# Kernel tuning notes

Hardware: AMD Instinct MI355X
Metric: run time of the kernel (lower is better)

The kernel has to match this reference:

```python
import jax, jax.numpy as jnp
import numpy as np

B, T, F = 256, 512, 256
H, C = 1024, 128


def setup_inputs() -> dict:
    key = jax.random.key(0)
    ks = jax.random.split(key, 12)
    s = 0.05
    return {
        "y": jax.random.normal(ks[0], (B, T, F), jnp.float32),
        "W_ih1": jax.random.normal(ks[1], (4 * H, F), jnp.float32) * s,
        "W_hh1": jax.random.normal(ks[2], (4 * H, H), jnp.float32) * s,
        "b_ih1": jax.random.normal(ks[3], (4 * H,), jnp.float32) * s,
        "b_hh1": jax.random.normal(ks[4], (4 * H,), jnp.float32) * s,
        "W_ih2": jax.random.normal(ks[5], (4 * H, H), jnp.float32) * s,
        "W_hh2": jax.random.normal(ks[6], (4 * H, H), jnp.float32) * s,
        "b_ih2": jax.random.normal(ks[7], (4 * H,), jnp.float32) * s,
        "b_hh2": jax.random.normal(ks[8], (4 * H,), jnp.float32) * s,
        "W_out": jax.random.normal(ks[9], (C, H), jnp.float32) * s,
        "b_out": jax.random.normal(ks[10], (C,), jnp.float32) * s,
    }


def _lstm_cell(x, h, c, W_ih, W_hh, b_ih, b_hh):
    # PyTorch LSTMCell: gates ordered i, f, g, o
    gates = x @ W_ih.T + b_ih + h @ W_hh.T + b_hh
    i, f, g, o = jnp.split(gates, 4, axis=-1)
    i, f, o = jax.nn.sigmoid(i), jax.nn.sigmoid(f), jax.nn.sigmoid(o)
    g = jnp.tanh(g)
    c_new = f * c + i * g
    h_new = o * jnp.tanh(c_new)
    return h_new, c_new


def reference(y, W_ih1, W_hh1, b_ih1, b_hh1, W_ih2, W_hh2, b_ih2, b_hh2, W_out, b_out):
    n = y.shape[0]
    z = jnp.zeros((n, H), jnp.float32)

    def step(carry, x_t):
        h1, c1, h2, c2 = carry
        h1, c1 = _lstm_cell(x_t, h1, c1, W_ih1, W_hh1, b_ih1, b_hh1)
        h2, c2 = _lstm_cell(h1, h2, c2, W_ih2, W_hh2, b_ih2, b_hh2)
        h2 = jnp.tanh(h2)  # note: tanh'd h2 is also the recurrent state, as in source
        out = jax.nn.relu(h2 @ W_out.T + b_out)
        return (h1, c1, h2, c2), out

    xs = jnp.transpose(y, (1, 0, 2))  # [T, B, F]
    _, outs = jax.lax.scan(step, (z, z, z, z), xs)
    # return_sequences=False -> last timestep output [B, C]
    return outs[-1]
```

## Files before the change

### kernel.cpp

```cpp
#include <hip/hip_runtime.h>
#include <hip/hip_bf16.h>

#define Bb 256
#define Tt 512
#define Ff 256
#define Hh 1024
#define Cc 128
#define NBLK 256
#define NTHR 512

typedef __bf16 bf16;
typedef bf16 bf16x8 __attribute__((ext_vector_type(8)));
typedef float f32x4 __attribute__((ext_vector_type(4)));

#define MFMA(a, b, c) __builtin_amdgcn_mfma_f32_16x16x32_bf16(a, b, c, 0, 0, 0)

struct SMem {
    bf16x8 w[2 * 64 * 64];
    bf16 hstage[256 * 8];
};

__device__ __forceinline__ float fsig(float x) {
    x = fminf(30.f, fmaxf(-30.f, x));
    return __builtin_amdgcn_rcpf(1.f + __expf(-x));
}
__device__ __forceinline__ float ftanh(float x) {
    x = fminf(15.f, fmaxf(-15.f, x));
    float e = __expf(2.f * x);
    return (e - 1.f) * __builtin_amdgcn_rcpf(e + 1.f);
}

#define STX4_SC1(p, v) \
    asm volatile("global_store_dwordx4 %0, %1, off sc1" :: "v"(p), "v"(v) : "memory")
#define LDX4_PLAIN(dst, base, OFF) \
    asm volatile("global_load_dwordx4 %0, %1, off offset:" #OFF : "=v"(dst) : "v"(base))

#define ISSUE_CHUNK(B0, B1, P0, P1) do { \
    LDX4_PLAIN(B0[0], (P0), 0);   LDX4_PLAIN(B0[1], (P0), 64);  LDX4_PLAIN(B0[2], (P0), 128); LDX4_PLAIN(B0[3], (P0), 192); \
    LDX4_PLAIN(B0[4], (P0), 256); LDX4_PLAIN(B0[5], (P0), 320); LDX4_PLAIN(B0[6], (P0), 384); LDX4_PLAIN(B0[7], (P0), 448); \
    LDX4_PLAIN(B1[0], (P1), 0);   LDX4_PLAIN(B1[1], (P1), 64);  LDX4_PLAIN(B1[2], (P1), 128); LDX4_PLAIN(B1[3], (P1), 192); \
    LDX4_PLAIN(B1[4], (P1), 256); LDX4_PLAIN(B1[5], (P1), 320); LDX4_PLAIN(B1[6], (P1), 384); LDX4_PLAIN(B1[7], (P1), 448); \
} while (0)

#define WAITV(N, B0, B1) \
    asm volatile("s_waitcnt vmcnt(" #N ")" : \
        "+v"(B0[0]), "+v"(B0[1]), "+v"(B0[2]), "+v"(B0[3]), \
        "+v"(B0[4]), "+v"(B0[5]), "+v"(B0[6]), "+v"(B0[7]), \
        "+v"(B1[0]), "+v"(B1[1]), "+v"(B1[2]), "+v"(B1[3]), \
        "+v"(B1[4]), "+v"(B1[5]), "+v"(B1[6]), "+v"(B1[7]) :: "memory")

#define MFMA8(ABASE, B0, B1) do { \
    _Pragma("unroll") \
    for (int _i = 0; _i < 8; ++_i) { \
        bf16x8 _a0 = wA0[((ABASE) + _i) * 64 + lane]; \
        bf16x8 _a1 = wA1[((ABASE) + _i) * 64 + lane]; \
        bf16x8 _b0 = __builtin_bit_cast(bf16x8, B0[_i]); \
        bf16x8 _b1 = __builtin_bit_cast(bf16x8, B1[_i]); \
        acc00 = MFMA(_a0, _b0, acc00); acc10 = MFMA(_a1, _b0, acc10); \
        acc01 = MFMA(_a0, _b1, acc01); acc11 = MFMA(_a1, _b1, acc11); \
    } \
} while (0)

__device__ __forceinline__ const bf16* phsel(int idx, const bf16* p, const bf16* q) {
    return ((idx < 4) ? p : q) + (idx & 3) * 256;
}

__device__ __forceinline__ void mm32(const bf16x8* __restrict__ wA0, const bf16x8* __restrict__ wA1,
                                     int abase, const bf16* p0, const bf16* p1, int lane, int rot,
                                     f32x4& acc00, f32x4& acc01, f32x4& acc10, f32x4& acc11)
{
    f32x4 bx0[8], bx1[8], by0[8], by1[8];
    const int c0 = rot & 3, c1 = (rot + 1) & 3, c2 = (rot + 2) & 3, c3 = (rot + 3) & 3;
    const bf16* a0 = p0 + c0 * 256; const bf16* a1 = p1 + c0 * 256;
    const bf16* b0 = p0 + c1 * 256; const bf16* b1 = p1 + c1 * 256;
    const bf16* d0 = p0 + c2 * 256; const bf16* d1 = p1 + c2 * 256;
    const bf16* e0 = p0 + c3 * 256; const bf16* e1 = p1 + c3 * 256;
    asm volatile("s_waitcnt vmcnt(0)" ::: "memory");
    ISSUE_CHUNK(bx0, bx1, a0, a1);
    ISSUE_CHUNK(by0, by1, b0, b1);
    WAITV(16, bx0, bx1);
    MFMA8(abase + c0 * 8, bx0, bx1);
    ISSUE_CHUNK(bx0, bx1, d0, d1);
    WAITV(16, by0, by1);
    MFMA8(abase + c1 * 8, by0, by1);
    ISSUE_CHUNK(by0, by1, e0, e1);
    WAITV(16, bx0, bx1);
    MFMA8(abase + c2 * 8, bx0, bx1);
    WAITV(0, by0, by1);
    MFMA8(abase + c3 * 8, by0, by1);
}

__device__ __forceinline__ void mm64(const bf16x8* __restrict__ wA0, const bf16x8* __restrict__ wA1,
                                     const bf16* p0, const bf16* p1,
                                     const bf16* q0, const bf16* q1, int lane, int rot,
                                     f32x4& acc00, f32x4& acc01, f32x4& acc10, f32x4& acc11)
{
    f32x4 bx0[8], bx1[8], by0[8], by1[8];
    const int i0 = rot & 7, i1 = (rot + 1) & 7, i2 = (rot + 2) & 7, i3 = (rot + 3) & 7;
    const int i4 = (rot + 4) & 7, i5 = (rot + 5) & 7, i6 = (rot + 6) & 7, i7 = (rot + 7) & 7;
    asm volatile("s_waitcnt vmcnt(0)" ::: "memory");
    { const bf16* u0 = phsel(i0, p0, q0); const bf16* u1 = phsel(i0, p1, q1); ISSUE_CHUNK(bx0, bx1, u0, u1); }
    { const bf16* u0 = phsel(i1, p0, q0); const bf16* u1 = phsel(i1, p1, q1); ISSUE_CHUNK(by0, by1, u0, u1); }
    WAITV(16, bx0, bx1); MFMA8(i0 * 8, bx0, bx1);
    { const bf16* u0 = phsel(i2, p0, q0); const bf16* u1 = phsel(i2, p1, q1); ISSUE_CHUNK(bx0, bx1, u0, u1); }
    WAITV(16, by0, by1); MFMA8(i1 * 8, by0, by1);
    { const bf16* u0 = phsel(i3, p0, q0); const bf16* u1 = phsel(i3, p1, q1); ISSUE_CHUNK(by0, by1, u0, u1); }
    WAITV(16, bx0, bx1); MFMA8(i2 * 8, bx0, bx1);
    { const bf16* u0 = phsel(i4, p0, q0); const bf16* u1 = phsel(i4, p1, q1); ISSUE_CHUNK(bx0, bx1, u0, u1); }
    WAITV(16, by0, by1); MFMA8(i3 * 8, by0, by1);
    { const bf16* u0 = phsel(i5, p0, q0); const bf16* u1 = phsel(i5, p1, q1); ISSUE_CHUNK(by0, by1, u0, u1); }
    WAITV(16, bx0, bx1); MFMA8(i4 * 8, bx0, bx1);
    { const bf16* u0 = phsel(i6, p0, q0); const bf16* u1 = phsel(i6, p1, q1); ISSUE_CHUNK(bx0, bx1, u0, u1); }
    WAITV(16, by0, by1); MFMA8(i5 * 8, by0, by1);
    { const bf16* u0 = phsel(i7, p0, q0); const bf16* u1 = phsel(i7, p1, q1); ISSUE_CHUNK(by0, by1, u0, u1); }
    WAITV(16, bx0, bx1); MFMA8(i6 * 8, bx0, bx1);
    WAITV(0, by0, by1); MFMA8(i7 * 8, by0, by1);
}

__device__ __forceinline__ float lstm_cell(const f32x4& acc, const f32x4& bq, float& c, bool extra_tanh) {
    float iv = fsig(acc[0] + bq[0]);
    float fv = fsig(acc[1] + bq[1]);
    float gv = ftanh(acc[2] + bq[2]);
    float ov = fsig(acc[3] + bq[3]);
    float cn = fv * c + iv * gv;
    c = cn;
    float h = ov * ftanh(cn);
    return extra_tanh ? ftanh(h) : h;
}

__device__ __forceinline__ void epilogue(SMem& sm, f32x4 acc00, f32x4 acc01, f32x4 acc10, f32x4 acc11,
                                         const f32x4& bq0, const f32x4& bq1,
                                         float creg[4], bf16* hdst, int hu0, bool extra_tanh) {
    const int tid = threadIdx.x;
    const int lane = tid & 63, wv = tid >> 6, quad = lane >> 4, l15 = lane & 15;
    const int b0 = wv * 32 + l15;
    float h00 = lstm_cell(acc00, bq0, creg[0], extra_tanh);
    float h01 = lstm_cell(acc01, bq0, creg[1], extra_tanh);
    float h10 = lstm_cell(acc10, bq1, creg[2], extra_tanh);
    float h11 = lstm_cell(acc11, bq1, creg[3], extra_tanh);
    sm.hstage[b0 * 8 + quad]            = (bf16)h00;
    sm.hstage[(b0 + 16) * 8 + quad]     = (bf16)h01;
    sm.hstage[b0 * 8 + 4 + quad]        = (bf16)h10;
    sm.hstage[(b0 + 16) * 8 + 4 + quad] = (bf16)h11;
    __syncthreads();
    if (tid < 256) {
        bf16x8 v = *(const bf16x8*)&sm.hstage[tid * 8];
        bf16* p = hdst + (size_t)tid * Hh + hu0;
        f32x4 pv = __builtin_bit_cast(f32x4, v);
        STX4_SC1(p, pv);
    }
}

__global__ void __launch_bounds__(NTHR, 2)
lstm_kernel(const float* __restrict__ y,
            const float* __restrict__ Wih1, const float* __restrict__ Whh1,
            const float* __restrict__ bih1, const float* __restrict__ bhh1,
            const float* __restrict__ Wih2, const float* __restrict__ Whh2,
            const float* __restrict__ bih2, const float* __restrict__ bhh2,
            const float* __restrict__ Wout, const float* __restrict__ bout,
            float* __restrict__ out,
            bf16* __restrict__ h1b0, bf16* __restrict__ h1b1,
            bf16* __restrict__ h2b0, bf16* __restrict__ h2b1,
            char* __restrict__ ctl)
{
    __shared__ SMem sm;
    const int tid = threadIdx.x;
    const int bid = blockIdx.x;
    const bool isL2 = bid >= 128;
    const int hu0 = (bid & 127) * 8;
    const int KI = isL2 ? 64 : 40;
    const int lane = tid & 63;
    const int wv = tid >> 6;
    const int quad = lane >> 4;
    const int l15 = lane & 15;
    const int rot4 = bid & 3;
    const int rot8 = bid & 7;

    unsigned* boot   = (unsigned*)ctl;
    unsigned* arrive = (unsigned*)(ctl + 2048);

    f32x4 bq0, bq1;
    #pragma unroll
    for (int r = 0; r < 4; ++r) {
        int g0 = r * Hh + hu0 + quad;
        int g1 = r * Hh + hu0 + 4 + quad;
        bq0[r] = isL2 ? (bih2[g0] + bhh2[g0]) : (bih1[g0] + bhh1[g0]);
        bq1[r] = isL2 ? (bih2[g1] + bhh2[g1]) : (bih1[g1] + bhh1[g1]);
    }
    for (int slot = tid; slot < 2 * KI * 64; slot += NTHR) {
        int mt = slot / (KI * 64);
        int ki = (slot / 64) % KI;
        int ln = slot & 63;
        int local = ln & 15;
        int k = ki * 32 + (ln >> 4) * 8;
        int gate = local & 3;
        int j = mt * 4 + (local >> 2);
        int grow = gate * Hh + hu0 + j;
        const float* src;
        if (!isL2) src = (k < Ff) ? (Wih1 + (size_t)grow * Ff + k) : (Whh1 + (size_t)grow * Hh + (k - Ff));
        else       src = (k < Hh) ? (Wih2 + (size_t)grow * Hh + k) : (Whh2 + (size_t)grow * Hh + (k - Hh));
        bf16x8 fr;
        #pragma unroll
        for (int e = 0; e < 8; ++e) fr[e] = (bf16)src[e];
        sm.w[slot] = fr;
    }
    float creg[4] = {0.f, 0.f, 0.f, 0.f};
    __syncthreads();

    if (tid == 0)
        __hip_atomic_store(&boot[bid], 1u, __ATOMIC_RELAXED, __HIP_MEMORY_SCOPE_AGENT);
    if (tid < 64) {
        for (;;) {
            int ok = 1;
            #pragma unroll
            for (int j = 0; j < 4; ++j)
                ok &= (__hip_atomic_load(&boot[tid * 4 + j], __ATOMIC_RELAXED,
                                         __HIP_MEMORY_SCOPE_AGENT) >= 1u);
            if (__all(ok)) break;
            __builtin_amdgcn_s_sleep(4);
        }
    }
    __syncthreads();

    const int nb0 = wv * 32 + l15;
    const bf16x8* wA0 = sm.w;
    const bf16x8* wA1 = sm.w + KI * 64;

    for (int s = 0; s <= Tt; ++s) {
        const int t = isL2 ? (s - 1) : s;
        const bool active = isL2 ? (s >= 1) : (s < Tt);
        f32x4 acc00 = {0,0,0,0}, acc01 = {0,0,0,0}, acc10 = {0,0,0,0}, acc11 = {0,0,0,0};

        if (!isL2 && active) {
            const f32x4* x0v = (const f32x4*)(y + ((size_t)nb0 * Tt + t) * Ff) + quad * 2;
            const f32x4* x1v = x0v + (size_t)16 * Tt * (Ff / 4);
            #pragma unroll
            for (int ki = 0; ki < 8; ++ki) {
                bf16x8 a0 = wA0[ki * 64 + lane];
                bf16x8 a1 = wA1[ki * 64 + lane];
                f32x4 u0 = x0v[ki * 8], u1 = x0v[ki * 8 + 1];
                f32x4 w0 = x1v[ki * 8], w1 = x1v[ki * 8 + 1];
                bf16x8 b0, b1;
                #pragma unroll
                for (int e = 0; e < 4; ++e) {
                    b0[e] = (bf16)u0[e]; b0[4 + e] = (bf16)u1[e];
                    b1[e] = (bf16)w0[e]; b1[4 + e] = (bf16)w1[e];
                }
                acc00 = MFMA(a0, b0, acc00); acc10 = MFMA(a1, b0, acc10);
                acc01 = MFMA(a0, b1, acc01); acc11 = MFMA(a1, b1, acc11);
            }
        }

        if (s >= 1) {
            const unsigned e = (unsigned)s;
            if (tid < 64) {
                for (;;) {
                    int ok = 1;
                    #pragma unroll
                    for (int j = 0; j < 4; ++j)
                        ok &= (__hip_atomic_load(&arrive[tid * 4 + j], __ATOMIC_RELAXED,
                                                 __HIP_MEMORY_SCOPE_AGENT) >= e);
                    if (__all(ok)) break;
                    __builtin_amdgcn_s_sleep(2);
                }
                __builtin_amdgcn_fence(__ATOMIC_ACQUIRE, "agent");
            }
            __syncthreads();
        }

        if (active) {
            const bf16* h1rd = ((s - 1) & 1) ? h1b1 : h1b0;
            if (!isL2) {
                if (t > 0) {
                    const bf16* p0 = h1rd + (size_t)nb0 * Hh + quad * 8;
                    mm32(wA0, wA1, 8, p0, p0 + 16 * Hh, lane, rot4, acc00, acc01, acc10, acc11);
                }
                epilogue(sm, acc00, acc01, acc10, acc11, bq0, bq1, creg,
                         (t & 1) ? h1b1 : h1b0, hu0, false);
            } else {
                const bf16* p0 = h1rd + (size_t)nb0 * Hh + quad * 8;
                if (t > 0) {
                    const bf16* h2rd = (s & 1) ? h2b1 : h2b0;
                    const bf16* q0 = h2rd + (size_t)nb0 * Hh + quad * 8;
                    mm64(wA0, wA1, p0, p0 + 16 * Hh, q0, q0 + 16 * Hh, lane, rot8,
                         acc00, acc01, acc10, acc11);
                } else {
                    mm32(wA0, wA1, 0, p0, p0 + 16 * Hh, lane, rot4, acc00, acc01, acc10, acc11);
                }
                epilogue(sm, acc00, acc01, acc10, acc11, bq0, bq1, creg,
                         (t & 1) ? h2b1 : h2b0, hu0, true);
            }
        }

        __syncthreads();
        if (tid == 0)
            __hip_atomic_store(&arrive[bid], (unsigned)(s + 1), __ATOMIC_RELAXED,
                               __HIP_MEMORY_SCOPE_AGENT);
    }

    {
        const unsigned e = (unsigned)(Tt + 1);
        if (tid < 64) {
            for (;;) {
                int ok = 1;
                #pragma unroll
                for (int j = 0; j < 4; ++j)
                    ok &= (__hip_atomic_load(&arrive[tid * 4 + j], __ATOMIC_RELAXED,
                                             __HIP_MEMORY_SCOPE_AGENT) >= e);
                if (__all(ok)) break;
                __builtin_amdgcn_s_sleep(2);
            }
            __builtin_amdgcn_fence(__ATOMIC_ACQUIRE, "agent");
        }
        __syncthreads();
    }

    if (bid < 16) {
        const int bb = bid * 16 + l15;
        const float* ap = Wout + (size_t)(wv * 16 + l15) * Hh + quad * 8;
        const bf16* bp = h2b1 + (size_t)bb * Hh + quad * 8;
        f32x4 acc = {0,0,0,0};
        #pragma unroll 4
        for (int ki = 0; ki < 32; ++ki) {
            bf16x8 a;
            #pragma unroll
            for (int e = 0; e < 8; ++e) a[e] = (bf16)ap[ki * 32 + e];
            bf16x8 b = *(const bf16x8*)(bp + ki * 32);
            acc = MFMA(a, b, acc);
        }
        #pragma unroll
        for (int r = 0; r < 4; ++r) {
            int orow = wv * 16 + quad * 4 + r;
            float v = acc[r] + bout[orow];
            out[(size_t)bb * Cc + orow] = fmaxf(v, 0.f);
        }
    }
}

extern "C" void kernel_launch(void* const* d_in, const int* in_sizes, int n_in,
                              void* d_out, int out_size, void* d_ws, size_t ws_size,
                              hipStream_t stream) {
    const float* y    = (const float*)d_in[0];
    const float* Wih1 = (const float*)d_in[1];
    const float* Whh1 = (const float*)d_in[2];
    const float* bih1 = (const float*)d_in[3];
    const float* bhh1 = (const float*)d_in[4];
    const float* Wih2 = (const float*)d_in[5];
    const float* Whh2 = (const float*)d_in[6];
    const float* bih2 = (const float*)d_in[7];
    const float* bhh2 = (const float*)d_in[8];
    const float* Wout = (const float*)d_in[9];
    const float* bout = (const float*)d_in[10];
    float* out = (float*)d_out;

    char* wsteal = (char*)d_in[2] + ((size_t)4 * Hh * Hh * sizeof(float) - 4 * 524288);
    bf16* h1b0 = (bf16*)(wsteal);
    bf16* h1b1 = (bf16*)(wsteal + 1 * 524288);
    bf16* h2b0 = (bf16*)(wsteal + 2 * 524288);
    bf16* h2b1 = (bf16*)(wsteal + 3 * 524288);

    char* ctl = (char*)d_ws;
    hipMemsetAsync(ctl, 0, 32768, stream);

    void* args[] = { &y, &Wih1, &Whh1, &bih1, &bhh1, &Wih2, &Whh2, &bih2, &bhh2,
                     &Wout, &bout, &out, &h1b0, &h1b1, &h2b0, &h2b1, &ctl };
    hipLaunchCooperativeKernel((void*)lstm_kernel, dim3(NBLK), dim3(NTHR), args, 0, stream);
}
```

Baseline: 18.56 ms.

## Use per-XCD leader barrier and sc0 loads to cut global barrier polling

Each block reads its XCC ID and elects one leader block per XCD with an atomic CAS. Only leaders poll all 256 arrival counters each step; the other blocks spin on a single per-XCD flag that the leader sets after its acquire fence. The hidden-state loads switch from plain loads to sc0 loads, and the final output-layer h2 read does the same, apparently relying on the leader's acquire to make data visible across the XCD. This cuts atomic polling traffic but adds an extra hop of latency per step, and its memory-visibility correctness rests on cache-coherence assumptions.

```diff
diff --git a/kernel.cpp b/kernel.cpp
--- a/kernel.cpp
+++ b/kernel.cpp
@@ -18,6 +18,8 @@
 struct SMem {
     bf16x8 w[2 * 64 * 64];
     bf16 hstage[256 * 8];
+    int leader;
+    int xcd;
 };
 
 __device__ __forceinline__ float fsig(float x) {
@@ -32,14 +34,14 @@
 
 #define STX4_SC1(p, v) \
     asm volatile("global_store_dwordx4 %0, %1, off sc1" :: "v"(p), "v"(v) : "memory")
-#define LDX4_PLAIN(dst, base, OFF) \
-    asm volatile("global_load_dwordx4 %0, %1, off offset:" #OFF : "=v"(dst) : "v"(base))
+#define LDX4_SC0(dst, base, OFF) \
+    asm volatile("global_load_dwordx4 %0, %1, off offset:" #OFF " sc0" : "=v"(dst) : "v"(base))
 
 #define ISSUE_CHUNK(B0, B1, P0, P1) do { \
-    LDX4_PLAIN(B0[0], (P0), 0);   LDX4_PLAIN(B0[1], (P0), 64);  LDX4_PLAIN(B0[2], (P0), 128); LDX4_PLAIN(B0[3], (P0), 192); \
-    LDX4_PLAIN(B0[4], (P0), 256); LDX4_PLAIN(B0[5], (P0), 320); LDX4_PLAIN(B0[6], (P0), 384); LDX4_PLAIN(B0[7], (P0), 448); \
-    LDX4_PLAIN(B1[0], (P1), 0);   LDX4_PLAIN(B1[1], (P1), 64);  LDX4_PLAIN(B1[2], (P1), 128); LDX4_PLAIN(B1[3], (P1), 192); \
-    LDX4_PLAIN(B1[4], (P1), 256); LDX4_PLAIN(B1[5], (P1), 320); LDX4_PLAIN(B1[6], (P1), 384); LDX4_PLAIN(B1[7], (P1), 448); \
+    LDX4_SC0(B0[0], (P0), 0);   LDX4_SC0(B0[1], (P0), 64);  LDX4_SC0(B0[2], (P0), 128); LDX4_SC0(B0[3], (P0), 192); \
+    LDX4_SC0(B0[4], (P0), 256); LDX4_SC0(B0[5], (P0), 320); LDX4_SC0(B0[6], (P0), 384); LDX4_SC0(B0[7], (P0), 448); \
+    LDX4_SC0(B1[0], (P1), 0);   LDX4_SC0(B1[1], (P1), 64);  LDX4_SC0(B1[2], (P1), 128); LDX4_SC0(B1[3], (P1), 192); \
+    LDX4_SC0(B1[4], (P1), 256); LDX4_SC0(B1[5], (P1), 320); LDX4_SC0(B1[6], (P1), 384); LDX4_SC0(B1[7], (P1), 448); \
 } while (0)
 
 #define WAITV(N, B0, B1) \
@@ -178,6 +180,16 @@
 
     unsigned* boot   = (unsigned*)ctl;
     unsigned* arrive = (unsigned*)(ctl + 2048);
+    unsigned* lead   = (unsigned*)(ctl + 4096);
+    unsigned* invf   = (unsigned*)(ctl + 8192);
+
+    if (tid == 0) {
+        unsigned x;
+        asm volatile("s_getreg_b32 %0, hwreg(HW_REG_XCC_ID, 0, 32)" : "=s"(x));
+        x &= 7u;
+        sm.xcd = (int)x;
+        sm.leader = (atomicCAS(&lead[x], 0u, 1u) == 0u) ? 1 : 0;
+    }
 
     f32x4 bq0, bq1;
     #pragma unroll
@@ -222,6 +234,8 @@
     }
     __syncthreads();
 
+    const int isLead = sm.leader;
+    const int myxcd  = sm.xcd;
     const int nb0 = wv * 32 + l15;
     const bf16x8* wA0 = sm.w;
     const bf16x8* wA1 = sm.w + KI * 64;
@@ -253,17 +267,29 @@
 
         if (s >= 1) {
             const unsigned e = (unsigned)s;
-            if (tid < 64) {
-                for (;;) {
-                    int ok = 1;
-                    #pragma unroll
-                    for (int j = 0; j < 4; ++j)
-                        ok &= (__hip_atomic_load(&arrive[tid * 4 + j], __ATOMIC_RELAXED,
-                                                 __HIP_MEMORY_SCOPE_AGENT) >= e);
-                    if (__all(ok)) break;
-                    __builtin_amdgcn_s_sleep(2);
-                }
-                __builtin_amdgcn_fence(__ATOMIC_ACQUIRE, "agent");
+            if (isLead) {
+                if (tid < 64) {
+                    for (;;) {
+                        int ok = 1;
+                        #pragma unroll
+                        for (int j = 0; j < 4; ++j)
+                            ok &= (__hip_atomic_load(&arrive[tid * 4 + j], __ATOMIC_RELAXED,
+                                                     __HIP_MEMORY_SCOPE_AGENT) >= e);
+                        if (__all(ok)) break;
+                        __builtin_amdgcn_s_sleep(1);
+                    }
+                    __builtin_amdgcn_fence(__ATOMIC_ACQUIRE, "agent");
+                    asm volatile("s_waitcnt vmcnt(0)" ::: "memory");
+                    if (tid == 0)
+                        __hip_atomic_store(&invf[myxcd * 32], e, __ATOMIC_RELAXED,
+                                           __HIP_MEMORY_SCOPE_AGENT);
+                }
+            } else {
+                if (tid < 64) {
+                    while (__hip_atomic_load(&invf[myxcd * 32], __ATOMIC_RELAXED,
+                                             __HIP_MEMORY_SCOPE_AGENT) < e)
+                        __builtin_amdgcn_s_sleep(1);
+                }
             }
             __syncthreads();
         }
@@ -300,17 +326,29 @@
 
     {
         const unsigned e = (unsigned)(Tt + 1);
-        if (tid < 64) {
-            for (;;) {
-                int ok = 1;
-                #pragma unroll
-                for (int j = 0; j < 4; ++j)
-                    ok &= (__hip_atomic_load(&arrive[tid * 4 + j], __ATOMIC_RELAXED,
-                                             __HIP_MEMORY_SCOPE_AGENT) >= e);
-                if (__all(ok)) break;
-                __builtin_amdgcn_s_sleep(2);
+        if (isLead) {
+            if (tid < 64) {
+                for (;;) {
+                    int ok = 1;
+                    #pragma unroll
+                    for (int j = 0; j < 4; ++j)
+                        ok &= (__hip_atomic_load(&arrive[tid * 4 + j], __ATOMIC_RELAXED,
+                                                 __HIP_MEMORY_SCOPE_AGENT) >= e);
+                    if (__all(ok)) break;
+                    __builtin_amdgcn_s_sleep(1);
+                }
+                __builtin_amdgcn_fence(__ATOMIC_ACQUIRE, "agent");
+                asm volatile("s_waitcnt vmcnt(0)" ::: "memory");
+                if (tid == 0)
+                    __hip_atomic_store(&invf[myxcd * 32], e, __ATOMIC_RELAXED,
+                                       __HIP_MEMORY_SCOPE_AGENT);
             }
-            __builtin_amdgcn_fence(__ATOMIC_ACQUIRE, "agent");
+        } else {
+            if (tid < 64) {
+                while (__hip_atomic_load(&invf[myxcd * 32], __ATOMIC_RELAXED,
+                                         __HIP_MEMORY_SCOPE_AGENT) < e)
+                    __builtin_amdgcn_s_sleep(1);
+            }
         }
         __syncthreads();
     }
@@ -325,7 +363,10 @@
             bf16x8 a;
             #pragma unroll
             for (int e = 0; e < 8; ++e) a[e] = (bf16)ap[ki * 32 + e];
-            bf16x8 b = *(const bf16x8*)(bp + ki * 32);
+            f32x4 braw;
+            LDX4_SC0(braw, (bp + ki * 32), 0);
+            asm volatile("s_waitcnt vmcnt(0)" ::: "memory");
+            bf16x8 b = __builtin_bit_cast(bf16x8, braw);
             acc = MFMA(a, b, acc);
         }
         #pragma unroll
```

Result: faster. 16.82 ms (-9.4%).
